# Optimization experiments

Measured on AMD Instinct MI355X. Metric: run time of the kernel, lower is better.

Reference implementation:

```python
import jax, jax.numpy as jnp
from jax import lax
import numpy as np

# Geometry fixed by __init__ (see shape_source)
UP = 2          # up_factor[0]
DOWN = 2        # down_factor[0]
PAD_LO = 11
PAD_HI = 10
SLOPE = 0.2
GAIN = np.sqrt(2.0).astype(np.float32)


def _kaiser_beta(atten):
    if atten > 50:
        return 0.1102 * (atten - 8.7)
    if atten > 21:
        return 0.5842 * (atten - 21.0) ** 0.4 + 0.07886 * (atten - 21.0)
    return 0.0


def _firwin(numtaps, cutoff, width, fs):
    # numpy re-implementation of scipy.signal.firwin(numtaps, cutoff, width=width, fs=fs)
    nyq = fs / 2.0
    atten = 2.285 * (numtaps - 1) * np.pi * (width / nyq) + 7.95  # kaiser_atten
    beta = _kaiser_beta(atten)
    m = np.arange(numtaps) - (numtaps - 1) / 2.0
    fc = cutoff / nyq
    h = fc * np.sinc(fc * m) * np.kaiser(numtaps, beta)
    h = h / h.sum()  # unity DC gain (pass_zero scaling)
    return h.astype(np.float32)


def _depthwise_conv1d(x, f, axis, stride=1, lhs_dilation=1, padding=(0, 0)):
    """Depthwise 1D FIR along spatial `axis` (2 or 3) of NCHW tensor.
    Filter is flipped (true convolution, as in upfirdn2d)."""
    C = x.shape[1]
    k = f.shape[0]
    fr = f[::-1]
    if axis == 2:
        kern = jnp.broadcast_to(fr.reshape(1, 1, k, 1), (C, 1, k, 1))
        strides, ld, pads = (stride, 1), (lhs_dilation, 1), [padding, (0, 0)]
    else:
        kern = jnp.broadcast_to(fr.reshape(1, 1, 1, k), (C, 1, 1, k))
        strides, ld, pads = (1, stride), (1, lhs_dilation), [(0, 0), padding]
    return lax.conv_general_dilated(
        x, kern, window_strides=strides, padding=pads, lhs_dilation=ld,
        dimension_numbers=('NCHW', 'OIHW', 'NCHW'), feature_group_count=C)


def setup_inputs() -> dict:
    key = jax.random.key(0)
    k1, k2 = jax.random.split(key)
    x = jax.random.normal(k1, (32, 128, 64, 64), dtype=jnp.float32)
    bias = jax.random.normal(k2, (128,), dtype=jnp.float32) * 0.1
    # up filter: numtaps=12, cutoff=in_cutoff=28, width=2*in_half_width=8, fs=tmp_sr=128
    up_filter = jnp.asarray(_firwin(12, 28.0, 8.0, 128.0))
    # down filter: numtaps=12, cutoff=out_cutoff=28, width=2*out_half_width=8, fs=128
    down_filter = jnp.asarray(_firwin(12, 28.0, 8.0, 128.0))
    return {"x": x, "bias": bias, "up_filter": up_filter, "down_filter": down_filter}


def reference(x, bias, up_filter, down_filter):
    # filtered_lrelu reference: upfirdn2d(up, fu, gain=up**2) -> bias -> lrelu*sqrt(2) -> upfirdn2d(down, fd)
    # Zero-insertion upsampling fused via lhs_dilation; dilated length is H*UP-(UP-1),
    # so the trailing UP-1 zeros of the nominal H*UP upsampled signal move into pad_hi.
    fu = up_filter * UP  # gain up per separable pass -> up**2 total
    pad = (PAD_LO, PAD_HI + UP - 1)
    y = _depthwise_conv1d(x, fu, axis=2, lhs_dilation=UP, padding=pad)
    y = _depthwise_conv1d(y, fu, axis=3, lhs_dilation=UP, padding=pad)  # [B,C,138,138]
    y = y + bias[None, :, None, None]
    y = jnp.where(y >= 0, y, SLOPE * y) * GAIN
    y = _depthwise_conv1d(y, down_filter, axis=2, stride=DOWN)
    y = _depthwise_conv1d(y, down_filter, axis=3, stride=DOWN)  # [B,C,64,64]
    return y
```

## Files before the change

### kernel.cpp

```cpp
#include <hip/hip_runtime.h>


#define NT 640
#define GAIN 1.41421356237309504880f
#define C1 (0.6f * GAIN)
#define C2 (0.4f * GAIN)

#define ZROWS 74
#define ZSTRIDE 84
#define ZPAD 8
#define YWSTRIDE 68

#define ZB_OFF 0
#define YW_OFF (ZROWS * ZSTRIDE)
#define LDS_FLOATS (YW_OFF + ZROWS * YWSTRIDE)

__device__ __forceinline__ float sload(float v) {
    return __uint_as_float(__builtin_amdgcn_readfirstlane(__float_as_uint(v)));
}

__global__ __launch_bounds__(NT, 8) void fused_upfirdn_lrelu(
    const float* __restrict__ x,
    const float* __restrict__ bias,
    const float* __restrict__ upf,
    const float* __restrict__ dnf,
    float* __restrict__ out)
{
    extern __shared__ float lds[];
    float* zb = lds + ZB_OFF;
    float* yw = lds + YW_OFF;

    const int t = threadIdx.x;
    const int bid = blockIdx.x;
    const int s = bid >> 1;
    const int o0 = (bid & 1) << 5;
    const int c = s & 127;

    float fu[12], fd[12];
#pragma unroll
    for (int j = 0; j < 12; ++j) {
        fu[j] = sload(2.0f * upf[j]);
        fd[j] = sload(dnf[j]);
    }
    const float bv = sload(bias[c]);

    const float* xg = x + (size_t)s * 4096;
    float* outg = out + (size_t)s * 4096;

    if (t < 304) {
        const int k = t >> 4;
        const int c4 = (t & 15) << 2;
        const int rbase = o0 - 5 + 2 * k;
        float4 xv[7];
#pragma unroll
        for (int d = 0; d < 7; ++d) {
            const int r = rbase + d;
            if (r >= 0 && r <= 63)
                xv[d] = *reinterpret_cast<const float4*>(xg + r * 64 + c4);
            else
                xv[d] = make_float4(0.f, 0.f, 0.f, 0.f);
        }
        float a0[4] = {0,0,0,0}, a1[4] = {0,0,0,0}, b0[4] = {0,0,0,0}, b1[4] = {0,0,0,0};
#pragma unroll
        for (int d = 0; d < 6; ++d) {
            const float w0 = fu[2 * (5 - d)], w1 = fu[2 * (5 - d) + 1];
            a0[0] += w0 * xv[d].x; a0[1] += w0 * xv[d].y; a0[2] += w0 * xv[d].z; a0[3] += w0 * xv[d].w;
            a1[0] += w1 * xv[d].x; a1[1] += w1 * xv[d].y; a1[2] += w1 * xv[d].z; a1[3] += w1 * xv[d].w;
        }
#pragma unroll
        for (int d = 1; d < 7; ++d) {
            const float w0 = fu[2 * (6 - d)], w1 = fu[2 * (6 - d) + 1];
            b0[0] += w0 * xv[d].x; b0[1] += w0 * xv[d].y; b0[2] += w0 * xv[d].z; b0[3] += w0 * xv[d].w;
            b1[0] += w1 * xv[d].x; b1[1] += w1 * xv[d].y; b1[2] += w1 * xv[d].z; b1[3] += w1 * xv[d].w;
        }
        float* zr = zb + (4 * k) * ZSTRIDE + ZPAD + c4;
        *reinterpret_cast<float4*>(zr)               = make_float4(a0[0], a0[1], a0[2], a0[3]);
        *reinterpret_cast<float4*>(zr + ZSTRIDE)     = make_float4(a1[0], a1[1], a1[2], a1[3]);
        if (k < 18) {
            *reinterpret_cast<float4*>(zr + 2 * ZSTRIDE) = make_float4(b0[0], b0[1], b0[2], b0[3]);
            *reinterpret_cast<float4*>(zr + 3 * ZSTRIDE) = make_float4(b1[0], b1[1], b1[2], b1[3]);
        }
    } else {
        for (int pt = t - 304; pt < 370; pt += 336) {
            const int rl = pt / 5;
            const int p = pt - rl * 5;
            const int col = (p < 2) ? (p << 2) : (72 + ((p - 2) << 2));
            *reinterpret_cast<float4*>(zb + rl * ZSTRIDE + col) = make_float4(0.f, 0.f, 0.f, 0.f);
        }
    }
    __syncthreads();

    {
        const int cg = t / 80;
        const int il = t - cg * 80;
        if (il < ZROWS) {
            const float* zr = zb + il * ZSTRIDE + (cg << 3);
            float zv[24];
#pragma unroll
            for (int q = 0; q < 6; ++q) {
                const float4 v = *reinterpret_cast<const float4*>(zr + (q << 2));
                zv[4 * q] = v.x; zv[4 * q + 1] = v.y; zv[4 * q + 2] = v.z; zv[4 * q + 3] = v.w;
            }
            float acc[8] = {0, 0, 0, 0, 0, 0, 0, 0};
#pragma unroll
            for (int v = 0; v < 13; ++v) {
                float a0 = bv, a1 = bv;
#pragma unroll
                for (int tt = 0; tt < 6; ++tt) {
                    const float zz = zv[v + 8 - tt];
                    a0 += fu[2 * tt]     * zz;
                    a1 += fu[2 * tt + 1] * zz;
                }
                const float y0 = C1 * a0 + C2 * fabsf(a0);
                const float y1 = C1 * a1 + C2 * fabsf(a1);
#pragma unroll
                for (int e = 0; e < 8; ++e) {
                    const int j0 = 2 * e + 11 - 2 * v;
                    const int j1 = 2 * e + 10 - 2 * v;
                    if (j0 >= 0 && j0 <= 11) acc[e] += fd[j0] * y0;
                    if (j1 >= 0 && j1 <= 11) acc[e] += fd[j1] * y1;
                }
            }
            float* wr = yw + il * YWSTRIDE + (cg << 3);
            *reinterpret_cast<float4*>(wr)     = make_float4(acc[0], acc[1], acc[2], acc[3]);
            *reinterpret_cast<float4*>(wr + 4) = make_float4(acc[4], acc[5], acc[6], acc[7]);
        }
    }
    __syncthreads();

    if (t < 128) {
        const int eg = t >> 4;
        const int col4 = (t & 15) << 2;
        const float* wr = yw + (eg << 3) * YWSTRIDE + col4;
        float acc[4][4] = {{0,0,0,0},{0,0,0,0},{0,0,0,0},{0,0,0,0}};
#pragma unroll
        for (int r = 0; r < 18; ++r) {
            const float4 v = *reinterpret_cast<const float4*>(wr + r * YWSTRIDE);
#pragma unroll
            for (int e = 0; e < 4; ++e) {
                if (r >= 2 * e && r <= 2 * e + 11) {
                    const float ww = fd[11 - r + 2 * e];
                    acc[e][0] += ww * v.x; acc[e][1] += ww * v.y;
                    acc[e][2] += ww * v.z; acc[e][3] += ww * v.w;
                }
            }
        }
#pragma unroll
        for (int e = 0; e < 4; ++e)
            *reinterpret_cast<float4*>(outg + (o0 + (eg << 2) + e) * 64 + col4) =
                make_float4(acc[e][0], acc[e][1], acc[e][2], acc[e][3]);
    }
}

extern "C" void kernel_launch(void* const* d_in, const int* in_sizes, int n_in,
                              void* d_out, int out_size, void* d_ws, size_t ws_size,
                              hipStream_t stream) {
    const float* x    = (const float*)d_in[0];
    const float* bias = (const float*)d_in[1];
    const float* upf  = (const float*)d_in[2];
    const float* dnf  = (const float*)d_in[3];
    float* out = (float*)d_out;

    const int n_blocks = 32 * 128 * 2;
    const size_t lds_bytes = (size_t)LDS_FLOATS * sizeof(float);
    hipLaunchKernelGGL(fused_upfirdn_lrelu, dim3(n_blocks), dim3(NT),
                       lds_bytes, stream, x, bias, upf, dnf, out);
}
```

Measured before the change: 83.30 us.

## Split each plane into four 16-row tiles and process two rows per thread

Each block now covers 16 output rows of a plane instead of 32, using 256 threads instead of 640, and the grid grows to four blocks per plane. In the middle horizontal pass, each thread handles two z rows at once with float2 values, so the filter weights and loop overhead are shared across both rows. The goal is more independent work per thread, smaller blocks and better scheduling. The cost is more halo recomputation at tile edges (42 upsampled rows per 16 outputs versus 74 per 32) and more registers per thread.

```diff
diff --git a/kernel.cpp b/kernel.cpp
--- a/kernel.cpp
+++ b/kernel.cpp
@@ -1,15 +1,16 @@
 #include <hip/hip_runtime.h>
 
 
-#define NT 640
+#define NT 256
 #define GAIN 1.41421356237309504880f
 #define C1 (0.6f * GAIN)
 #define C2 (0.4f * GAIN)
 
-#define ZROWS 74
+#define ZROWS 42
 #define ZSTRIDE 84
 #define ZPAD 8
 #define YWSTRIDE 68
+#define RPAIR 21
 
 #define ZB_OFF 0
 #define YW_OFF (ZROWS * ZSTRIDE)
@@ -19,7 +20,7 @@
     return __uint_as_float(__builtin_amdgcn_readfirstlane(__float_as_uint(v)));
 }
 
-__global__ __launch_bounds__(NT, 8) void fused_upfirdn_lrelu(
+__global__ __launch_bounds__(NT, 6) void fused_upfirdn_lrelu(
     const float* __restrict__ x,
     const float* __restrict__ bias,
     const float* __restrict__ upf,
@@ -32,8 +33,8 @@
 
     const int t = threadIdx.x;
     const int bid = blockIdx.x;
-    const int s = bid >> 1;
-    const int o0 = (bid & 1) << 5;
+    const int s = bid >> 2;
+    const int o0 = (bid & 3) << 4;
     const int c = s & 127;
 
     float fu[12], fd[12];
@@ -47,7 +48,7 @@
     const float* xg = x + (size_t)s * 4096;
     float* outg = out + (size_t)s * 4096;
 
-    if (t < 304) {
+    if (t < 176) {
         const int k = t >> 4;
         const int c4 = (t & 15) << 2;
         const int rbase = o0 - 5 + 2 * k;
@@ -76,12 +77,12 @@
         float* zr = zb + (4 * k) * ZSTRIDE + ZPAD + c4;
         *reinterpret_cast<float4*>(zr)               = make_float4(a0[0], a0[1], a0[2], a0[3]);
         *reinterpret_cast<float4*>(zr + ZSTRIDE)     = make_float4(a1[0], a1[1], a1[2], a1[3]);
-        if (k < 18) {
+        if (k < 10) {
             *reinterpret_cast<float4*>(zr + 2 * ZSTRIDE) = make_float4(b0[0], b0[1], b0[2], b0[3]);
             *reinterpret_cast<float4*>(zr + 3 * ZSTRIDE) = make_float4(b1[0], b1[1], b1[2], b1[3]);
         }
     } else {
-        for (int pt = t - 304; pt < 370; pt += 336) {
+        for (int pt = t - 176; pt < 210; pt += 80) {
             const int rl = pt / 5;
             const int p = pt - rl * 5;
             const int col = (p < 2) ? (p << 2) : (72 + ((p - 2) << 2));
@@ -91,44 +92,56 @@
     __syncthreads();
 
     {
-        const int cg = t / 80;
-        const int il = t - cg * 80;
-        if (il < ZROWS) {
-            const float* zr = zb + il * ZSTRIDE + (cg << 3);
-            float zv[24];
+        const int cg = t / 24;
+        const int r  = t - cg * 24;
+        if (cg < 8 && r < RPAIR) {
+            const float* zrA = zb + r * ZSTRIDE + (cg << 3);
+            const float* zrB = zrA + RPAIR * ZSTRIDE;
+            float2 zv[24];
 #pragma unroll
             for (int q = 0; q < 6; ++q) {
-                const float4 v = *reinterpret_cast<const float4*>(zr + (q << 2));
-                zv[4 * q] = v.x; zv[4 * q + 1] = v.y; zv[4 * q + 2] = v.z; zv[4 * q + 3] = v.w;
+                const float4 va = *reinterpret_cast<const float4*>(zrA + (q << 2));
+                const float4 vb = *reinterpret_cast<const float4*>(zrB + (q << 2));
+                zv[4 * q + 0] = make_float2(va.x, vb.x);
+                zv[4 * q + 1] = make_float2(va.y, vb.y);
+                zv[4 * q + 2] = make_float2(va.z, vb.z);
+                zv[4 * q + 3] = make_float2(va.w, vb.w);
             }
-            float acc[8] = {0, 0, 0, 0, 0, 0, 0, 0};
+            float2 acc[8];
+#pragma unroll
+            for (int e = 0; e < 8; ++e) acc[e] = make_float2(0.f, 0.f);
 #pragma unroll
             for (int v = 0; v < 13; ++v) {
-                float a0 = bv, a1 = bv;
+                float2 a0 = make_float2(bv, bv), a1 = make_float2(bv, bv);
 #pragma unroll
                 for (int tt = 0; tt < 6; ++tt) {
-                    const float zz = zv[v + 8 - tt];
-                    a0 += fu[2 * tt]     * zz;
-                    a1 += fu[2 * tt + 1] * zz;
+                    const float2 zz = zv[v + 8 - tt];
+                    const float w0 = fu[2 * tt], w1 = fu[2 * tt + 1];
+                    a0.x += w0 * zz.x; a0.y += w0 * zz.y;
+                    a1.x += w1 * zz.x; a1.y += w1 * zz.y;
                 }
-                const float y0 = C1 * a0 + C2 * fabsf(a0);
-                const float y1 = C1 * a1 + C2 * fabsf(a1);
+                float2 y0, y1;
+                y0.x = C1 * a0.x + C2 * fabsf(a0.x); y0.y = C1 * a0.y + C2 * fabsf(a0.y);
+                y1.x = C1 * a1.x + C2 * fabsf(a1.x); y1.y = C1 * a1.y + C2 * fabsf(a1.y);
 #pragma unroll
                 for (int e = 0; e < 8; ++e) {
                     const int j0 = 2 * e + 11 - 2 * v;
                     const int j1 = 2 * e + 10 - 2 * v;
-                    if (j0 >= 0 && j0 <= 11) acc[e] += fd[j0] * y0;
-                    if (j1 >= 0 && j1 <= 11) acc[e] += fd[j1] * y1;
+                    if (j0 >= 0 && j0 <= 11) { acc[e].x += fd[j0] * y0.x; acc[e].y += fd[j0] * y0.y; }
+                    if (j1 >= 0 && j1 <= 11) { acc[e].x += fd[j1] * y1.x; acc[e].y += fd[j1] * y1.y; }
                 }
             }
-            float* wr = yw + il * YWSTRIDE + (cg << 3);
-            *reinterpret_cast<float4*>(wr)     = make_float4(acc[0], acc[1], acc[2], acc[3]);
-            *reinterpret_cast<float4*>(wr + 4) = make_float4(acc[4], acc[5], acc[6], acc[7]);
+            float* wrA = yw + r * YWSTRIDE + (cg << 3);
+            float* wrB = wrA + RPAIR * YWSTRIDE;
+            *reinterpret_cast<float4*>(wrA)     = make_float4(acc[0].x, acc[1].x, acc[2].x, acc[3].x);
+            *reinterpret_cast<float4*>(wrA + 4) = make_float4(acc[4].x, acc[5].x, acc[6].x, acc[7].x);
+            *reinterpret_cast<float4*>(wrB)     = make_float4(acc[0].y, acc[1].y, acc[2].y, acc[3].y);
+            *reinterpret_cast<float4*>(wrB + 4) = make_float4(acc[4].y, acc[5].y, acc[6].y, acc[7].y);
         }
     }
     __syncthreads();
 
-    if (t < 128) {
+    if (t < 64) {
         const int eg = t >> 4;
         const int col4 = (t & 15) << 2;
         const float* wr = yw + (eg << 3) * YWSTRIDE + col4;
@@ -161,7 +174,7 @@
     const float* dnf  = (const float*)d_in[3];
     float* out = (float*)d_out;
 
-    const int n_blocks = 32 * 128 * 2;
+    const int n_blocks = 32 * 128 * 4;
     const size_t lds_bytes = (size_t)LDS_FLOATS * sizeof(float);
     hipLaunchKernelGGL(fused_upfirdn_lrelu, dim3(n_blocks), dim3(NT),
                        lds_bytes, stream, x, bias, upf, dnf, out);
```

New measurement: 84.03 us. About the same (+0.9%).
